# Performance work log

Hardware: AMD Instinct MI355X
Metric: run time of the kernel (lower is better)

## Reference

```python
import jax, jax.numpy as jnp
import numpy as np
from jax import lax

DN = ('NCHW', 'OIHW', 'NCHW')

def conv(x, w, b):
    y = lax.conv_general_dilated(x, w, (1, 1), 'VALID', dimension_numbers=DN)
    return y + b[None, :, None, None]

def maxpool2(x):
    return lax.reduce_window(x, -jnp.inf, lax.max, (1, 1, 2, 2), (1, 1, 2, 2), 'VALID')

def setup_inputs() -> dict:
    key = jax.random.key(0)
    ks = jax.random.split(key, 16)
    s = 0.05
    return {
        'x': jax.random.normal(ks[0], (8192, 1, 28, 28), jnp.float32),
        'kf_w1': jax.random.normal(ks[1], (8, 1, 7, 7), jnp.float32) * s,
        'kf_b1': jax.random.normal(ks[2], (8,), jnp.float32) * s,
        'kf_w2': jax.random.normal(ks[3], (10, 8, 5, 5), jnp.float32) * s,
        'kf_b2': jax.random.normal(ks[4], (10,), jnp.float32) * s,
        'kf_fc1_w': jax.random.normal(ks[5], (32, 90), jnp.float32) * s,
        'kf_fc1_b': jax.random.normal(ks[6], (32,), jnp.float32) * s,
        'kf_fc2_w': jax.random.normal(ks[7], (40, 32), jnp.float32) * s,
        'kf_fc2_b': jax.random.normal(ks[8], (40,), jnp.float32) * s,
        'conv2_w': jax.random.normal(ks[9], (20, 10, 5, 5), jnp.float32) * s,
        'conv2_b': jax.random.normal(ks[10], (20,), jnp.float32) * s,
        'fc1_w': jax.random.normal(ks[11], (50, 320), jnp.float32) * s,
        'fc1_b': jax.random.normal(ks[12], (50,), jnp.float32) * s,
        'fc2_w': jax.random.normal(ks[13], (10, 50), jnp.float32) * s,
        'fc2_b': jax.random.normal(ks[14], (10,), jnp.float32) * s,
    }

def _forward(x, kf_w1, kf_b1, kf_w2, kf_b2, kf_fc1_w, kf_fc1_b, kf_fc2_w, kf_fc2_b,
             conv2_w, conv2_b, fc1_w, fc1_b, fc2_w, fc2_b):
    n = x.shape[0]
    # KernelFinder: conv7 -> pool -> relu -> conv5 -> pool -> relu
    f = jax.nn.relu(maxpool2(conv(x, kf_w1, kf_b1)))        # [N,8,11,11]
    f = jax.nn.relu(maxpool2(conv(f, kf_w2, kf_b2)))        # [N,10,3,3]
    f = f.reshape(n, 90)
    h = jax.nn.relu(f @ kf_fc1_w.T + kf_fc1_b)
    kernels = (h @ kf_fc2_w.T + kf_fc2_b).reshape(n, 10, 1, 2, 2)
    # per-sample dynamic conv: each image gets its own [10,1,2,2] kernel
    def one(img, k):
        return lax.conv_general_dilated(img[None], k, (1, 1), 'VALID',
                                        dimension_numbers=DN)[0]
    y = jax.vmap(one)(x, kernels)                           # [N,10,27,27]
    y = jax.nn.relu(maxpool2(y))                            # [N,10,13,13]
    # dropout2d is identity in eval mode
    y = jax.nn.relu(maxpool2(conv(y, conv2_w, conv2_b)))    # [N,20,4,4]
    y = y.reshape(n, 320)
    y = jax.nn.relu(y @ fc1_w.T + fc1_b)
    # F.dropout identity in eval
    y = y @ fc2_w.T + fc2_b
    return jax.nn.log_softmax(y, axis=1)

def reference(x, kf_w1, kf_b1, kf_w2, kf_b2, kf_fc1_w, kf_fc1_b, kf_fc2_w, kf_fc2_b,
              conv2_w, conv2_b, fc1_w, fc1_b, fc2_w, fc2_b):
    return _forward(x, kf_w1, kf_b1, kf_w2, kf_b2, kf_fc1_w, kf_fc1_b, kf_fc2_w,
                    kf_fc2_b, conv2_w, conv2_b, fc1_w, fc1_b, fc2_w, fc2_b)
```

## Files before the change

### kernel.cpp

```cpp
#include <hip/hip_runtime.h>
#include <math.h>

#define TPB 192

typedef __attribute__((ext_vector_type(8))) short bf16x8;
typedef __attribute__((ext_vector_type(4))) float f32x4;

#define OX    0
#define OXB   784
#define OC1B  2720
#define OY2   784
#define OF    3248
#define OH    3340
#define OK2   3372
#define OC2S  2720
#define OP3   0
#define OPF   320
#define OA1   420
#define OZ    472
#define SM_TOT 5024

#define W3U 0
#define W5U 9600
#define W7U 13184
#define WSU_TOT 14208

__device__ __forceinline__ unsigned short f2bf(float f) {
    unsigned int u = __float_as_uint(f);
    u += 0x7FFF + ((u >> 16) & 1);
    return (unsigned short)(u >> 16);
}

__device__ __forceinline__ float dppmax1(float v) {
    float o = __int_as_float(__builtin_amdgcn_mov_dpp(
        __float_as_int(v), 0xB1, 0xF, 0xF, true));
    return fmaxf(v, o);
}
__device__ __forceinline__ float dppmax8(float v) {
    float o = __int_as_float(__builtin_amdgcn_mov_dpp(
        __float_as_int(v), 0x128, 0xF, 0xF, true));
    return fmaxf(v, o);
}

__global__ void repack_w(const float* __restrict__ conv2_w,
                         const float* __restrict__ kf_w2,
                         const float* __restrict__ kf_w1,
                         unsigned short* __restrict__ ws)
{
    int i = blockIdx.x * blockDim.x + threadIdx.x;
    if (i < 9600) {
        int g = i / 640, rem = i % 640;
        int oc = rem >> 5, k = rem & 31;
        int kyp = g % 3, kx = g / 3;
        int kyip = k >> 4, ic = k & 15, ky = 2 * kyp + kyip;
        float v = 0.f;
        if (ic < 10 && ky < 5)
            v = conv2_w[(oc * 10 + ic) * 25 + ky * 5 + kx];
        ws[W3U + i] = f2bf(v);
    } else if (i < 13184) {
        int j = i - 9600;
        int s = j >> 9, rem = j & 511;
        int oc = rem >> 5, k = rem & 31;
        int tap = 4 * s + (k >> 3), ic = k & 7;
        float v = 0.f;
        if (oc < 10 && tap < 25)
            v = kf_w2[(oc * 8 + ic) * 25 + tap];
        ws[W5U + j] = f2bf(v);
    } else if (i < WSU_TOT) {
        int j = i - 13184;
        int s = j >> 9, oc = (j >> 5) & 15, k = j & 31;
        int ky = s * 4 + (k >> 3), kx = k & 7;
        float v = 0.f;
        if (oc < 8 && kx < 7 && ky < 7)
            v = kf_w1[oc * 49 + ky * 7 + kx];
        ws[W7U + j] = f2bf(v);
    }
}

__global__ __launch_bounds__(TPB) void fused_forward(
    const float* __restrict__ x,
    const float* __restrict__ kf_w1, const float* __restrict__ kf_b1,
    const float* __restrict__ kf_w2, const float* __restrict__ kf_b2,
    const float* __restrict__ kf_fc1_w, const float* __restrict__ kf_fc1_b,
    const float* __restrict__ kf_fc2_w, const float* __restrict__ kf_fc2_b,
    const float* __restrict__ conv2_w, const float* __restrict__ conv2_b,
    const float* __restrict__ fc1_w, const float* __restrict__ fc1_b,
    const float* __restrict__ fc2_w, const float* __restrict__ fc2_b,
    const unsigned short* __restrict__ wsu,
    float* __restrict__ out)
{
    __shared__ __align__(16) float sm[SM_TOT];
    const int tid = threadIdx.x;
    const int n = blockIdx.x;

    const int l  = tid & 63, wv = tid >> 6;
    const int lm = l & 15, lk = l >> 4;

    bf16x8 A7_0, A7_1;
    {
        const unsigned short* W7 = wsu + W7U;
        A7_0 = *(const bf16x8*)(W7 + lm * 32 + lk * 8);
        A7_1 = *(const bf16x8*)(W7 + 512 + lm * 32 + lk * 8);
    }
    float4 b1v = *(const float4*)(kf_b1 + (lk < 2 ? lk : 0) * 4);

    {
        const float4* xg = (const float4*)(x + (long long)n * 784);
        float4* d = (float4*)&sm[OX];
        for (int i = tid; i < 196; i += TPB) d[i] = xg[i];
    }
    __syncthreads();

    {
        unsigned short* xb = (unsigned short*)&sm[OXB];
        #pragma unroll
        for (int i = 0; i < 20; ++i) {
            int e = i * 192 + tid;
            int s = e / 960, rem = e - s * 960;
            int r = rem >> 5, m = rem & 31;
            int c = m + s;
            float v = (r < 28 && c < 28) ? sm[OX + r * 28 + c] : 0.f;
            xb[s * 968 + rem] = f2bf(v);
        }
    }
    __syncthreads();

    {
        const unsigned short* xb = (const unsigned short*)&sm[OXB];
        unsigned short* c1b = (unsigned short*)&sm[OC1B];
        for (int g = 0; g < 3; ++g) {
            #pragma unroll
            for (int j = 0; j < 4; ++j) {
                int t = wv * 4 + j;
                int C = 2 * t + (lm >> 3);
                int lr = lm & 7;
                int s = C & 3, q = C - s;
                f32x4 acc = {0.f, 0.f, 0.f, 0.f};
                #pragma unroll
                for (int s4 = 0; s4 < 2; ++s4) {
                    int rb = 8 * g + lr + s4 * 4 + lk;
                    rb = rb > 29 ? 29 : rb;
                    const unsigned short* p = xb + s * 968 + rb * 32 + q;
                    short4 lo = *(const short4*)p;
                    short4 hi = *(const short4*)(p + 4);
                    bf16x8 B;
                    B[0] = lo.x; B[1] = lo.y; B[2] = lo.z; B[3] = lo.w;
                    B[4] = hi.x; B[5] = hi.y; B[6] = hi.z; B[7] = hi.w;
                    acc = __builtin_amdgcn_mfma_f32_16x16x32_bf16(
                        s4 ? A7_1 : A7_0, B, acc, 0, 0, 0);
                }
                #pragma unroll
                for (int e = 0; e < 4; ++e) acc[e] = dppmax1(acc[e]);
                #pragma unroll
                for (int e = 0; e < 4; ++e) acc[e] = dppmax8(acc[e]);
                int pr = 4 * g + (lm >> 1);
                if ((lm & 1) == 0 && lm < 8 && lk < 2 && t < 11 && pr < 11) {
                    short4 w;
                    w.x = (short)f2bf(fmaxf(acc[0] + b1v.x, 0.f));
                    w.y = (short)f2bf(fmaxf(acc[1] + b1v.y, 0.f));
                    w.z = (short)f2bf(fmaxf(acc[2] + b1v.z, 0.f));
                    w.w = (short)f2bf(fmaxf(acc[3] + b1v.w, 0.f));
                    *(short4*)(c1b + pr * 96 + t * 8 + lk * 4) = w;
                }
            }
        }
    }
    __syncthreads();

    {
        int row = lm & 7;
        int colc = 2 * wv + (lm >> 3);
        int rowc = row > 5 ? 5 : row;
        const unsigned short* c1b = (const unsigned short*)&sm[OC1B];
        const char* W5 = (const char*)(wsu + W5U);
        f32x4 acc = {0.f, 0.f, 0.f, 0.f};
        #pragma unroll
        for (int s = 0; s < 7; ++s) {
            int tap = 4 * s + lk;
            int ky = (tap * 13) >> 6;
            int kx = tap - ky * 5;
            bf16x8 A = *(const bf16x8*)(W5 + s * 1024 + lm * 64 + lk * 16);
            bf16x8 B = *(const bf16x8*)(c1b + (rowc + ky) * 96 + (colc + kx) * 8);
            acc = __builtin_amdgcn_mfma_f32_16x16x32_bf16(A, B, acc, 0, 0, 0);
        }
        #pragma unroll
        for (int e = 0; e < 4; ++e) acc[e] = dppmax1(acc[e]);
        #pragma unroll
        for (int e = 0; e < 4; ++e) acc[e] = dppmax8(acc[e]);
        if ((lm & 1) == 0 && lm < 6 && lk < 3) {
            int py = lm >> 1, px = wv;
            float* f = &sm[OF];
            if (lk < 2) {
                float4 b2 = *(const float4*)(kf_b2 + lk * 4);
                f[(lk * 4 + 0) * 9 + py * 3 + px] = fmaxf(acc[0] + b2.x, 0.f);
                f[(lk * 4 + 1) * 9 + py * 3 + px] = fmaxf(acc[1] + b2.y, 0.f);
                f[(lk * 4 + 2) * 9 + py * 3 + px] = fmaxf(acc[2] + b2.z, 0.f);
                f[(lk * 4 + 3) * 9 + py * 3 + px] = fmaxf(acc[3] + b2.w, 0.f);
            } else {
                float2 b2 = *(const float2*)(kf_b2 + 8);
                f[8 * 9 + py * 3 + px] = fmaxf(acc[0] + b2.x, 0.f);
                f[9 * 9 + py * 3 + px] = fmaxf(acc[1] + b2.y, 0.f);
            }
        }
    }
    __syncthreads();

    if (tid < 32) {
        float acc = kf_fc1_b[tid];
        const float2* wr = (const float2*)&kf_fc1_w[tid * 90];
        const float2* ff = (const float2*)&sm[OF];
        for (int i = 0; i < 45; ++i) {
            float2 wv2 = wr[i], fv = ff[i];
            acc = fmaf(wv2.x, fv.x, acc);
            acc = fmaf(wv2.y, fv.y, acc);
        }
        sm[OH + tid] = fmaxf(acc, 0.f);
    }
    if (tid < 40) {
        float acc = kf_fc2_b[tid];
        const float4* wr = (const float4*)&kf_fc2_w[tid * 32];
        const float4* hh = (const float4*)&sm[OH];
        #pragma unroll
        for (int i = 0; i < 8; ++i) {
            float4 wv2 = wr[i], hv = hh[i];
            acc = fmaf(wv2.x, hv.x, acc);
            acc = fmaf(wv2.y, hv.y, acc);
            acc = fmaf(wv2.z, hv.z, acc);
            acc = fmaf(wv2.w, hv.w, acc);
        }
        sm[OK2 + tid] = acc;
    }
    if (tid >= 64) {
        float4* z4 = (float4*)&sm[OY2];
        for (int i = tid - 64; i < 468; i += 128) z4[i] = float4{0.f, 0.f, 0.f, 0.f};
    }
    __syncthreads();

    if (tid < 120) {
        int oc = tid % 10, py = tid / 10;
        float4 kv = *(const float4*)&sm[OK2 + oc * 4];
        float k0 = kv.x, k1 = kv.y, k2 = kv.z, k3 = kv.w;
        const float* x0 = &sm[OX + 2 * py * 28];
        const float* x1 = x0 + 28;
        const float* x2 = x0 + 56;
        float2 q0 = *(const float2*)&x0[0];
        float2 q1 = *(const float2*)&x1[0];
        float2 q2 = *(const float2*)&x2[0];
        float A0 = q0.x, B0 = q0.y;
        float A1 = q1.x, B1 = q1.y;
        float A2 = q2.x, B2 = q2.y;
        unsigned short* y2 = (unsigned short*)&sm[OY2];
        #pragma unroll
        for (int j = 0; j < 12; ++j) {
            float2 r0 = *(const float2*)&x0[2 * j + 2];
            float2 r1 = *(const float2*)&x1[2 * j + 2];
            float2 r2v = *(const float2*)&x2[2 * j + 2];
            float C0 = r0.x, C1 = r1.x, C2 = r2v.x;
            float c00 = A0 * k0 + B0 * k1 + A1 * k2 + B1 * k3;
            float c01 = B0 * k0 + C0 * k1 + B1 * k2 + C1 * k3;
            float c10 = A1 * k0 + B1 * k1 + A2 * k2 + B2 * k3;
            float c11 = B1 * k0 + C1 * k1 + B2 * k2 + C2 * k3;
            float m = fmaxf(fmaxf(c00, c01), fmaxf(c10, c11));
            y2[py * 288 + j * 24 + oc] = f2bf(fmaxf(m, 0.f));
            A0 = C0; A1 = C1; A2 = C2;
            B0 = r0.y; B1 = r1.y; B2 = r2v.y;
        }
    }
    __syncthreads();

    if (wv < 2) {
        f32x4 a00 = {0.f, 0.f, 0.f, 0.f};
        f32x4 a01 = a00, a10 = a00, a11 = a00;
        const char* W3 = (const char*)(wsu + W3U);
        const int aoff0 = lm * 64 + lk * 16;
        const int oc1 = 16 + (lm < 4 ? lm : 3);
        const int aoff1 = oc1 * 64 + lk * 16;
        const int n0 = wv * 32 + lm;
        const int n1 = n0 + 16;
        const int kyip = l >> 5, icb = (lk & 1) * 8;
        const unsigned short* Y2 = (const unsigned short*)&sm[OY2];
        const int b0 = ((n0 >> 3) + kyip) * 288 + (n0 & 7) * 24 + icb;
        const int b1 = ((n1 >> 3) + kyip) * 288 + (n1 & 7) * 24 + icb;
        #pragma unroll
        for (int p = 0; p < 3; ++p) {
            #pragma unroll
            for (int kx = 0; kx < 5; ++kx) {
                const char* wa = W3 + (kx * 3 + p) * 1280;
                bf16x8 A0 = *(const bf16x8*)(wa + aoff0);
                bf16x8 A1 = *(const bf16x8*)(wa + aoff1);
                const int bo = p * 576 + kx * 24;
                bf16x8 B0 = *(const bf16x8*)(Y2 + b0 + bo);
                bf16x8 B1 = *(const bf16x8*)(Y2 + b1 + bo);
                a00 = __builtin_amdgcn_mfma_f32_16x16x32_bf16(A0, B0, a00, 0, 0, 0);
                a01 = __builtin_amdgcn_mfma_f32_16x16x32_bf16(A0, B1, a01, 0, 0, 0);
                a10 = __builtin_amdgcn_mfma_f32_16x16x32_bf16(A1, B0, a10, 0, 0, 0);
                a11 = __builtin_amdgcn_mfma_f32_16x16x32_bf16(A1, B1, a11, 0, 0, 0);
            }
        }
        float* C = &sm[OC2S];
        *(f32x4*)(C + n0 * 36 + lk * 4)      = a00;
        *(f32x4*)(C + n1 * 36 + lk * 4)      = a01;
        *(f32x4*)(C + n0 * 36 + 16 + lk * 4) = a10;
        *(f32x4*)(C + n1 * 36 + 16 + lk * 4) = a11;
    }
    __syncthreads();

    if (tid < 80) {
        int oc = tid % 20, py = tid / 20;
        float b = conv2_b[oc];
        const float* C = &sm[OC2S];
        #pragma unroll
        for (int px = 0; px < 4; ++px) {
            int n00 = (2 * py) * 8 + 2 * px;
            float c00 = C[n00 * 36 + oc];
            float c01 = C[(n00 + 1) * 36 + oc];
            float c10 = C[(n00 + 8) * 36 + oc];
            float c11 = C[(n00 + 9) * 36 + oc];
            float m = fmaxf(fmaxf(c00, c01), fmaxf(c10, c11)) + b;
            sm[OP3 + oc * 16 + py * 4 + px] = fmaxf(m, 0.f);
        }
    }
    __syncthreads();

    if (tid < 100) {
        int g = tid / 50, o = tid % 50;
        const float4* wr4 = (const float4*)&fc1_w[o * 320 + g * 160];
        const float4* pp4 = (const float4*)&sm[OP3 + g * 160];
        float acc = 0.f;
        for (int i = 0; i < 40; ++i) {
            float4 wv2 = wr4[i], pv = pp4[i];
            acc = fmaf(wv2.x, pv.x, acc);
            acc = fmaf(wv2.y, pv.y, acc);
            acc = fmaf(wv2.z, pv.z, acc);
            acc = fmaf(wv2.w, pv.w, acc);
        }
        sm[OPF + tid] = acc;
    }
    __syncthreads();

    if (tid < 50) {
        float acc = fc1_b[tid] + sm[OPF + tid] + sm[OPF + 50 + tid];
        sm[OA1 + tid] = fmaxf(acc, 0.f);
    }
    if (tid < 10) {
        float acc = fc2_b[tid];
        const float2* wr = (const float2*)&fc2_w[tid * 50];
        #pragma unroll
        for (int i = 0; i < 25; ++i) {
            float2 wv2 = wr[i];
            acc = fmaf(wv2.x, sm[OA1 + 2 * i], acc);
            acc = fmaf(wv2.y, sm[OA1 + 2 * i + 1], acc);
        }
        sm[OZ + tid] = acc;
    }
    if (tid < 10) {
        float m = sm[OZ + 0];
        #pragma unroll
        for (int i = 1; i < 10; ++i) m = fmaxf(m, sm[OZ + i]);
        float s = 0.f;
        #pragma unroll
        for (int i = 0; i < 10; ++i) s += expf(sm[OZ + i] - m);
        out[n * 10 + tid] = sm[OZ + tid] - m - logf(s);
    }
}

extern "C" void kernel_launch(void* const* d_in, const int* in_sizes, int n_in,
                              void* d_out, int out_size, void* d_ws, size_t ws_size,
                              hipStream_t stream) {
    const float* x        = (const float*)d_in[0];
    const float* kf_w1    = (const float*)d_in[1];
    const float* kf_b1    = (const float*)d_in[2];
    const float* kf_w2    = (const float*)d_in[3];
    const float* kf_b2    = (const float*)d_in[4];
    const float* kf_fc1_w = (const float*)d_in[5];
    const float* kf_fc1_b = (const float*)d_in[6];
    const float* kf_fc2_w = (const float*)d_in[7];
    const float* kf_fc2_b = (const float*)d_in[8];
    const float* conv2_w  = (const float*)d_in[9];
    const float* conv2_b  = (const float*)d_in[10];
    const float* fc1_w    = (const float*)d_in[11];
    const float* fc1_b    = (const float*)d_in[12];
    const float* fc2_w    = (const float*)d_in[13];
    const float* fc2_b    = (const float*)d_in[14];

    const int N = in_sizes[0] / 784;

    unsigned short* wsu = (unsigned short*)d_ws;
    repack_w<<<(WSU_TOT + 255) / 256, 256, 0, stream>>>(conv2_w, kf_w2, kf_w1, wsu);

    fused_forward<<<N, TPB, 0, stream>>>(
        x, kf_w1, kf_b1, kf_w2, kf_b2, kf_fc1_w, kf_fc1_b, kf_fc2_w, kf_fc2_b,
        conv2_w, conv2_b, fc1_w, fc1_b, fc2_w, fc2_b, wsu, (float*)d_out);
}
```

Baseline: 221.4 us.

## Widen block to four waves and redistribute per-stage work across them

New measurement: 220.2 us. About the same (-0.5%).

```diff
diff --git a/kernel.cpp b/kernel.cpp
--- a/kernel.cpp
+++ b/kernel.cpp
@@ -1,7 +1,7 @@
 #include <hip/hip_runtime.h>
 #include <math.h>
 
-#define TPB 192
+#define TPB 256
 
 typedef __attribute__((ext_vector_type(8))) short bf16x8;
 typedef __attribute__((ext_vector_type(4))) float f32x4;
@@ -16,8 +16,8 @@
 #define OC2S  2720
 #define OP3   0
 #define OPF   320
-#define OA1   420
-#define OZ    472
+#define OA1   520
+#define OZ    572
 #define SM_TOT 5024
 
 #define W3U 0
@@ -114,8 +114,8 @@
     {
         unsigned short* xb = (unsigned short*)&sm[OXB];
         #pragma unroll
-        for (int i = 0; i < 20; ++i) {
-            int e = i * 192 + tid;
+        for (int i = 0; i < 15; ++i) {
+            int e = i * 256 + tid;
             int s = e / 960, rem = e - s * 960;
             int r = rem >> 5, m = rem & 31;
             int c = m + s;
@@ -130,8 +130,8 @@
         unsigned short* c1b = (unsigned short*)&sm[OC1B];
         for (int g = 0; g < 3; ++g) {
             #pragma unroll
-            for (int j = 0; j < 4; ++j) {
-                int t = wv * 4 + j;
+            for (int j = 0; j < 3; ++j) {
+                int t = wv * 3 + j;
                 int C = 2 * t + (lm >> 3);
                 int lr = lm & 7;
                 int s = C & 3, q = C - s;
@@ -167,7 +167,7 @@
     }
     __syncthreads();
 
-    {
+    if (wv < 3) {
         int row = lm & 7;
         int colc = 2 * wv + (lm >> 3);
         int rowc = row > 5 ? 5 : row;
@@ -202,6 +202,9 @@
                 f[9 * 9 + py * 3 + px] = fmaxf(acc[1] + b2.y, 0.f);
             }
         }
+    } else {
+        float4* z4 = (float4*)&sm[OY2];
+        for (int i = l; i < 468; i += 64) z4[i] = float4{0.f, 0.f, 0.f, 0.f};
     }
     __syncthreads();
 
@@ -230,17 +233,14 @@
         }
         sm[OK2 + tid] = acc;
     }
-    if (tid >= 64) {
-        float4* z4 = (float4*)&sm[OY2];
-        for (int i = tid - 64; i < 468; i += 128) z4[i] = float4{0.f, 0.f, 0.f, 0.f};
-    }
-    __syncthreads();
-
-    if (tid < 120) {
-        int oc = tid % 10, py = tid / 10;
+    __syncthreads();
+
+    if (tid < 240) {
+        int oc = tid % 10, r = tid / 10;
+        int py = r % 12, hh = r / 12;
         float4 kv = *(const float4*)&sm[OK2 + oc * 4];
         float k0 = kv.x, k1 = kv.y, k2 = kv.z, k3 = kv.w;
-        const float* x0 = &sm[OX + 2 * py * 28];
+        const float* x0 = &sm[OX + 2 * py * 28 + 12 * hh];
         const float* x1 = x0 + 28;
         const float* x2 = x0 + 56;
         float2 q0 = *(const float2*)&x0[0];
@@ -251,7 +251,7 @@
         float A2 = q2.x, B2 = q2.y;
         unsigned short* y2 = (unsigned short*)&sm[OY2];
         #pragma unroll
-        for (int j = 0; j < 12; ++j) {
+        for (int j = 0; j < 6; ++j) {
             float2 r0 = *(const float2*)&x0[2 * j + 2];
             float2 r1 = *(const float2*)&x1[2 * j + 2];
             float2 r2v = *(const float2*)&x2[2 * j + 2];
@@ -261,21 +261,22 @@
             float c10 = A1 * k0 + B1 * k1 + A2 * k2 + B2 * k3;
             float c11 = B1 * k0 + C1 * k1 + B2 * k2 + C2 * k3;
             float m = fmaxf(fmaxf(c00, c01), fmaxf(c10, c11));
-            y2[py * 288 + j * 24 + oc] = f2bf(fmaxf(m, 0.f));
+            y2[py * 288 + (6 * hh + j) * 24 + oc] = f2bf(fmaxf(m, 0.f));
             A0 = C0; A1 = C1; A2 = C2;
             B0 = r0.y; B1 = r1.y; B2 = r2v.y;
         }
     }
     __syncthreads();
 
-    if (wv < 2) {
-        f32x4 a00 = {0.f, 0.f, 0.f, 0.f};
-        f32x4 a01 = a00, a10 = a00, a11 = a00;
+    {
+        const int mw = wv >> 1, npair = wv & 1;
+        f32x4 a0 = {0.f, 0.f, 0.f, 0.f};
+        f32x4 a1 = a0;
         const char* W3 = (const char*)(wsu + W3U);
-        const int aoff0 = lm * 64 + lk * 16;
-        const int oc1 = 16 + (lm < 4 ? lm : 3);
-        const int aoff1 = oc1 * 64 + lk * 16;
-        const int n0 = wv * 32 + lm;
+        int aoff;
+        if (mw == 0) aoff = lm * 64 + lk * 16;
+        else { int oc1 = 16 + (lm < 4 ? lm : 3); aoff = oc1 * 64 + lk * 16; }
+        const int n0 = npair * 32 + lm;
         const int n1 = n0 + 16;
         const int kyip = l >> 5, icb = (lk & 1) * 8;
         const unsigned short* Y2 = (const unsigned short*)&sm[OY2];
@@ -286,22 +287,17 @@
             #pragma unroll
             for (int kx = 0; kx < 5; ++kx) {
                 const char* wa = W3 + (kx * 3 + p) * 1280;
-                bf16x8 A0 = *(const bf16x8*)(wa + aoff0);
-                bf16x8 A1 = *(const bf16x8*)(wa + aoff1);
+                bf16x8 A = *(const bf16x8*)(wa + aoff);
                 const int bo = p * 576 + kx * 24;
                 bf16x8 B0 = *(const bf16x8*)(Y2 + b0 + bo);
                 bf16x8 B1 = *(const bf16x8*)(Y2 + b1 + bo);
-                a00 = __builtin_amdgcn_mfma_f32_16x16x32_bf16(A0, B0, a00, 0, 0, 0);
-                a01 = __builtin_amdgcn_mfma_f32_16x16x32_bf16(A0, B1, a01, 0, 0, 0);
-                a10 = __builtin_amdgcn_mfma_f32_16x16x32_bf16(A1, B0, a10, 0, 0, 0);
-                a11 = __builtin_amdgcn_mfma_f32_16x16x32_bf16(A1, B1, a11, 0, 0, 0);
+                a0 = __builtin_amdgcn_mfma_f32_16x16x32_bf16(A, B0, a0, 0, 0, 0);
+                a1 = __builtin_amdgcn_mfma_f32_16x16x32_bf16(A, B1, a1, 0, 0, 0);
             }
         }
         float* C = &sm[OC2S];
-        *(f32x4*)(C + n0 * 36 + lk * 4)      = a00;
-        *(f32x4*)(C + n1 * 36 + lk * 4)      = a01;
-        *(f32x4*)(C + n0 * 36 + 16 + lk * 4) = a10;
-        *(f32x4*)(C + n1 * 36 + 16 + lk * 4) = a11;
+        *(f32x4*)(C + n0 * 36 + mw * 16 + lk * 4) = a0;
+        *(f32x4*)(C + n1 * 36 + mw * 16 + lk * 4) = a1;
     }
     __syncthreads();
 
@@ -322,12 +318,12 @@
     }
     __syncthreads();
 
-    if (tid < 100) {
+    if (tid < 200) {
         int g = tid / 50, o = tid % 50;
-        const float4* wr4 = (const float4*)&fc1_w[o * 320 + g * 160];
-        const float4* pp4 = (const float4*)&sm[OP3 + g * 160];
+        const float4* wr4 = (const float4*)&fc1_w[o * 320 + g * 80];
+        const float4* pp4 = (const float4*)&sm[OP3 + g * 80];
         float acc = 0.f;
-        for (int i = 0; i < 40; ++i) {
+        for (int i = 0; i < 20; ++i) {
             float4 wv2 = wr4[i], pv = pp4[i];
             acc = fmaf(wv2.x, pv.x, acc);
             acc = fmaf(wv2.y, pv.y, acc);
@@ -339,7 +335,8 @@
     __syncthreads();
 
     if (tid < 50) {
-        float acc = fc1_b[tid] + sm[OPF + tid] + sm[OPF + 50 + tid];
+        float acc = fc1_b[tid] + sm[OPF + tid] + sm[OPF + 50 + tid]
+                  + sm[OPF + 100 + tid] + sm[OPF + 150 + tid];
         sm[OA1 + tid] = fmaxf(acc, 0.f);
     }
     if (tid < 10) {
```
